# Kernel optimization log

Measured on AMD Instinct MI355X. Metric: run time of the kernel, lower is better.

Reference implementation:

```python
import jax, jax.numpy as jnp
import numpy as np
from jax import lax

DIM = 192
HEADS = 4
HIDDEN = int(DIM * 2.66)  # 510
B, H, W = 2, 64, 64
EPS_LN = 1e-6
EPS_NORM = 1e-12


def conv1x1(x, w, b):
    # x: (b,c,h,w), w: (o,c), b: (o,)
    return jnp.einsum('bchw,oc->bohw', x, w) + b[None, :, None, None]


def dwconv3x3(x, w, b):
    # depthwise 3x3, SAME padding; w: (C,1,3,3)
    c = x.shape[1]
    y = lax.conv_general_dilated(x, w, window_strides=(1, 1), padding='SAME',
                                 feature_group_count=c,
                                 dimension_numbers=('NCHW', 'OIHW', 'NCHW'))
    return y + b[None, :, None, None]


def layernorm2d(x, w, b):
    mean = jnp.mean(x, axis=(2, 3), keepdims=True)
    var = jnp.mean((x - mean) ** 2, axis=(2, 3), keepdims=True)
    return (x - mean) / jnp.sqrt(var + EPS_LN) * w[None, :, None, None] + b[None, :, None, None]


def mdta(x, qkv_w, qkv_b, qkv_dw_w, qkv_dw_b, temperature, proj_w, proj_b):
    b, c, h, w = x.shape
    qkv = dwconv3x3(conv1x1(x, qkv_w, qkv_b), qkv_dw_w, qkv_dw_b)
    q, k, v = jnp.split(qkv, 3, axis=1)
    dh = c // HEADS
    q = q.reshape(b, HEADS, dh, h * w)
    k = k.reshape(b, HEADS, dh, h * w)
    v = v.reshape(b, HEADS, dh, h * w)
    # L2-normalize over per-head channel dim (axis=2), like F.normalize(dim=2)
    q = q / jnp.maximum(jnp.linalg.norm(q, axis=2, keepdims=True), EPS_NORM)
    k = k / jnp.maximum(jnp.linalg.norm(k, axis=2, keepdims=True), EPS_NORM)
    # spatial attention map: (b, heads, HW, HW)
    attn = jnp.einsum('bhcn,bhcm->bhnm', q, k) * temperature[None]  # temp (heads,1,1)
    attn = jax.nn.softmax(attn, axis=-1)
    out = jnp.einsum('bhnm,bhcm->bhcn', attn, v)  # (b,heads,dh,HW)
    out = out.reshape(b, c, h, w)
    return conv1x1(out, proj_w, proj_b)


def gdfn(x, pin_w, pin_b, dw_w, dw_b, pout_w, pout_b):
    y = dwconv3x3(conv1x1(x, pin_w, pin_b), dw_w, dw_b)
    y1, y2 = jnp.split(y, 2, axis=1)
    y = jax.nn.gelu(y1, approximate=False) * y2
    return conv1x1(y, pout_w, pout_b)


def setup_inputs() -> dict:
    key = jax.random.key(0)
    ks = jax.random.split(key, 8)
    s = 0.02
    return {
        'x': jax.random.normal(ks[0], (B, DIM, H, W), jnp.float32),
        'ln1_w': jnp.ones((DIM,), jnp.float32),
        'ln1_b': jnp.zeros((DIM,), jnp.float32),
        'qkv_w': jax.random.normal(ks[1], (DIM * 3, DIM), jnp.float32) * s,
        'qkv_b': jnp.zeros((DIM * 3,), jnp.float32),
        'qkv_dw_w': jax.random.normal(ks[2], (DIM * 3, 1, 3, 3), jnp.float32) * s,
        'qkv_dw_b': jnp.zeros((DIM * 3,), jnp.float32),
        'temperature': jnp.ones((HEADS, 1, 1), jnp.float32),
        'proj_w': jax.random.normal(ks[3], (DIM, DIM), jnp.float32) * s,
        'proj_b': jnp.zeros((DIM,), jnp.float32),
        'ln2_w': jnp.ones((DIM,), jnp.float32),
        'ln2_b': jnp.zeros((DIM,), jnp.float32),
        'pin_w': jax.random.normal(ks[4], (HIDDEN * 2, DIM), jnp.float32) * s,
        'pin_b': jnp.zeros((HIDDEN * 2,), jnp.float32),
        'gdfn_dw_w': jax.random.normal(ks[5], (HIDDEN * 2, 1, 3, 3), jnp.float32) * s,
        'gdfn_dw_b': jnp.zeros((HIDDEN * 2,), jnp.float32),
        'pout_w': jax.random.normal(ks[6], (DIM, HIDDEN), jnp.float32) * s,
        'pout_b': jnp.zeros((DIM,), jnp.float32),
    }


def reference(x, ln1_w, ln1_b, qkv_w, qkv_b, qkv_dw_w, qkv_dw_b, temperature,
              proj_w, proj_b, ln2_w, ln2_b, pin_w, pin_b, gdfn_dw_w, gdfn_dw_b,
              pout_w, pout_b):
    x = x + mdta(layernorm2d(x, ln1_w, ln1_b), qkv_w, qkv_b, qkv_dw_w, qkv_dw_b,
                 temperature, proj_w, proj_b)
    x = x + gdfn(layernorm2d(x, ln2_w, ln2_b), pin_w, pin_b, gdfn_dw_w, gdfn_dw_b,
                 pout_w, pout_b)
    return x
```

## Files before the change

### kernel.cpp

```cpp
#include <hip/hip_runtime.h>
#include <hip/hip_bf16.h>

typedef __bf16 bf16x8 __attribute__((ext_vector_type(8)));
typedef __bf16 bf16x4 __attribute__((ext_vector_type(4)));
typedef __bf16 bf16x2 __attribute__((ext_vector_type(2)));
typedef float f32x4 __attribute__((ext_vector_type(4)));

#define HW 4096
#define DIMC 192
#define DH 48
#define HIDC 510
#define LOG2E 1.44269504088896f

__global__ void wcvt4_kernel(const float* __restrict__ qkv_w, const float* __restrict__ proj_w,
                             const float* __restrict__ pin_w, const float* __restrict__ pout_w,
                             __bf16* __restrict__ wb_qkv, __bf16* __restrict__ wb_proj,
                             __bf16* __restrict__ wb_pin, __bf16* __restrict__ wb_pout) {
  int idx = blockIdx.x * 256 + threadIdx.x;
  if (idx < 110592) {
    wb_qkv[idx] = (__bf16)qkv_w[idx];
  } else if (idx < 147456) {
    int i = idx - 110592;
    wb_proj[i] = (__bf16)proj_w[i];
  } else if (idx < 343296) {
    int i = idx - 147456;
    wb_pin[i] = (__bf16)pin_w[i];
  } else if (idx < 441600) {
    int i = idx - 343296;
    int o = i >> 9, c = i & 511;
    wb_pout[i] = (c < HIDC) ? (__bf16)pout_w[o * HIDC + c] : (__bf16)0.f;
  }
}

__global__ __launch_bounds__(256) void ln_stats_kernel(const float* __restrict__ x, const float* __restrict__ w,
                                                       const float* __restrict__ b, float* __restrict__ sc,
                                                       float* __restrict__ sh) {
  int bc = blockIdx.x;
  int c = bc % DIMC;
  const float* row = x + (size_t)bc * HW;
  float s = 0.f, s2 = 0.f;
  for (int i = threadIdx.x * 4; i < HW; i += 1024) {
    f32x4 v = *(const f32x4*)&row[i];
    s += (v.x + v.y) + (v.z + v.w);
    s2 = fmaf(v.x, v.x, s2); s2 = fmaf(v.y, v.y, s2);
    s2 = fmaf(v.z, v.z, s2); s2 = fmaf(v.w, v.w, s2);
  }
  __shared__ float red[8];
  for (int off = 32; off; off >>= 1) { s += __shfl_down(s, off, 64); s2 += __shfl_down(s2, off, 64); }
  int wid = threadIdx.x >> 6;
  if ((threadIdx.x & 63) == 0) { red[wid] = s; red[4 + wid] = s2; }
  __syncthreads();
  if (threadIdx.x == 0) {
    s = red[0] + red[1] + red[2] + red[3];
    s2 = red[4] + red[5] + red[6] + red[7];
    float mean = s * (1.f / HW);
    float var = s2 * (1.f / HW) - mean * mean;
    float rstd = rsqrtf(var + 1e-6f);
    float scv = rstd * w[c];
    sc[bc] = scv;
    sh[bc] = b[c] - mean * scv;
  }
}

__global__ __launch_bounds__(256) void ln_apply_t_kernel(const float* __restrict__ x, const float* __restrict__ sc,
                                                         const float* __restrict__ sh, __bf16* __restrict__ Xt) {
  int n0 = blockIdx.x * 64, c0 = blockIdx.y * 32, b = blockIdx.z;
  int t = threadIdx.x;
  int n = t & 63, cs = c0 + (t >> 6) * 8;
  __bf16 ob[8];
#pragma unroll
  for (int cc = 0; cc < 8; ++cc) {
    int c = cs + cc;
    float v = fmaf(x[((size_t)(b * DIMC + c)) * HW + n0 + n], sc[b * DIMC + c], sh[b * DIMC + c]);
    ob[cc] = (__bf16)v;
  }
  *(bf16x8*)&Xt[((size_t)((b << 12) + n0 + n)) * DIMC + cs] = *(bf16x8*)ob;
}

__global__ __launch_bounds__(256) void gemm_kernel(const __bf16* __restrict__ A, const __bf16* __restrict__ Bt,
                                                   const float* __restrict__ bias, const float* __restrict__ res,
                                                   float* __restrict__ outf, __bf16* __restrict__ outb,
                                                   int O, int Cs, int mode) {
  __shared__ __align__(16) __bf16 Asub[64 * 72];
  __shared__ __align__(16) __bf16 Bsub[128 * 72];
  const int t = threadIdx.x;
  const int lane = t & 63, wv = t >> 6;
  const int q4 = lane >> 4, l16 = lane & 15;
  int o0 = blockIdx.y * 64;
  if (o0 + 64 > O) o0 = O - 64;
  const int ntot0 = blockIdx.x * 128;
  const int b = ntot0 >> 12;
  const int n_in_b0 = ntot0 & 4095;

  f32x4 acc[8];
#pragma unroll
  for (int nt = 0; nt < 8; ++nt) acc[nt] = (f32x4){0.f, 0.f, 0.f, 0.f};

  for (int c0 = 0; c0 < Cs; c0 += 64) {
    __syncthreads();
#pragma unroll
    for (int j = 0; j < 2; ++j) {
      int id = t + 256 * j;
      *(bf16x8*)&Asub[(id >> 3) * 72 + (id & 7) * 8] =
          *(const bf16x8*)&A[((size_t)(o0 + (id >> 3))) * Cs + c0 + (id & 7) * 8];
    }
    if (mode != 3) {
#pragma unroll
      for (int j = 0; j < 4; ++j) {
        int id = t + 256 * j;
        *(bf16x8*)&Bsub[(id >> 3) * 72 + (id & 7) * 8] =
            *(const bf16x8*)&Bt[((size_t)(ntot0 + (id >> 3))) * Cs + c0 + (id & 7) * 8];
      }
    } else {
      int cr = t >> 2, seg = t & 3;
      int cg = c0 + cr;
      __bf16 tmp[32];
      if (cg < HIDC) {
        const __bf16* gp = Bt + ((size_t)(b * HIDC + cg)) * HW + n_in_b0 + seg * 32;
#pragma unroll
        for (int j = 0; j < 4; ++j) *(bf16x8*)&tmp[8 * j] = *(const bf16x8*)&gp[8 * j];
      } else {
#pragma unroll
        for (int k = 0; k < 32; ++k) tmp[k] = (__bf16)0.f;
      }
#pragma unroll
      for (int k = 0; k < 32; ++k) Bsub[(seg * 32 + k) * 72 + cr] = tmp[k];
    }
    __syncthreads();
#pragma unroll
    for (int ks = 0; ks < 2; ++ks) {
      bf16x8 af = *(const bf16x8*)&Asub[(16 * wv + l16) * 72 + 32 * ks + 8 * q4];
#pragma unroll
      for (int nt = 0; nt < 8; ++nt) {
        bf16x8 bfr = *(const bf16x8*)&Bsub[(16 * nt + l16) * 72 + 32 * ks + 8 * q4];
        acc[nt] = __builtin_amdgcn_mfma_f32_16x16x32_bf16(af, bfr, acc[nt], 0, 0, 0);
      }
    }
  }

  float bvals[4];
#pragma unroll
  for (int r = 0; r < 4; ++r) bvals[r] = bias[o0 + 16 * wv + 4 * q4 + r];
#pragma unroll
  for (int nt = 0; nt < 8; ++nt) {
    int n_in_b = n_in_b0 + 16 * nt + l16;
#pragma unroll
    for (int r = 0; r < 4; ++r) {
      int o = o0 + 16 * wv + 4 * q4 + r;
      size_t addr = ((size_t)(b * O + o)) * HW + n_in_b;
      float v = acc[nt][r] + bvals[r];
      if (mode >= 2) { outf[addr] = v + res[addr]; }
      else if (mode == 0) { outf[addr] = v; }
      else { outb[addr] = (__bf16)v; }
    }
  }
}

__global__ __launch_bounds__(256) void dwconv_split_kernel(const __bf16* __restrict__ in, const float* __restrict__ w,
                                                           const float* __restrict__ bias,
                                                           __bf16* __restrict__ qdwb, __bf16* __restrict__ Vbf) {
  int bc = blockIdx.x;
  int b = bc / 576, ch = bc - b * 576;
  __shared__ float tile[66 * 68];
  for (int i = threadIdx.x; i < 66 * 68; i += 256) tile[i] = 0.f;
  __syncthreads();
  const __bf16* p = in + (size_t)bc * HW;
  for (int j = 0; j < 8; ++j) {
    int i = 2 * threadIdx.x + 512 * j;
    bf16x2 v = *(const bf16x2*)&p[i];
    int y = i >> 6, xx = i & 63;
    tile[(y + 1) * 68 + xx + 1] = (float)v.x;
    tile[(y + 1) * 68 + xx + 2] = (float)v.y;
  }
  __syncthreads();
  float w0 = w[ch * 9 + 0], w1 = w[ch * 9 + 1], w2 = w[ch * 9 + 2];
  float w3 = w[ch * 9 + 3], w4 = w[ch * 9 + 4], w5 = w[ch * 9 + 5];
  float w6 = w[ch * 9 + 6], w7 = w[ch * 9 + 7], w8 = w[ch * 9 + 8];
  float bb = bias[ch];
  __bf16* dst;
  if (ch < 384) dst = qdwb + ((size_t)(b * 384 + ch)) * HW;
  else {
    int c = ch - 384, h = c / DH, cc = c - h * DH;
    dst = Vbf + ((size_t)((b * 4 + h) * DH + cc)) * HW;
  }
  for (int j = 0; j < 8; ++j) {
    int i = 2 * threadIdx.x + 512 * j;
    int y = i >> 6, xx = i & 63;
    const float* tt = &tile[y * 68 + xx];
    float a = bb;
    a = fmaf(w0, tt[0], a);   a = fmaf(w1, tt[1], a);   a = fmaf(w2, tt[2], a);
    a = fmaf(w3, tt[68], a);  a = fmaf(w4, tt[69], a);  a = fmaf(w5, tt[70], a);
    a = fmaf(w6, tt[136], a); a = fmaf(w7, tt[137], a); a = fmaf(w8, tt[138], a);
    float a2 = bb;
    a2 = fmaf(w0, tt[1], a2);   a2 = fmaf(w1, tt[2], a2);   a2 = fmaf(w2, tt[3], a2);
    a2 = fmaf(w3, tt[69], a2);  a2 = fmaf(w4, tt[70], a2);  a2 = fmaf(w5, tt[71], a2);
    a2 = fmaf(w6, tt[137], a2); a2 = fmaf(w7, tt[138], a2); a2 = fmaf(w8, tt[139], a2);
    bf16x2 o = { (__bf16)a, (__bf16)a2 };
    *(bf16x2*)&dst[i] = o;
  }
}

__global__ __launch_bounds__(256) void gdfn_dw_gate_kernel(const __bf16* __restrict__ hid, const float* __restrict__ w,
                                                           const float* __restrict__ bias, __bf16* __restrict__ gate) {
  int blk = blockIdx.x;
  int b = blk / HIDC, j = blk - b * HIDC;
  __shared__ float t1[66 * 68];
  __shared__ float t2[66 * 68];
  for (int i = threadIdx.x; i < 66 * 68; i += 256) { t1[i] = 0.f; t2[i] = 0.f; }
  __syncthreads();
  const __bf16* p1 = hid + ((size_t)b * (2 * HIDC) + j) * HW;
  const __bf16* p2 = p1 + (size_t)HIDC * HW;
  for (int jj = 0; jj < 8; ++jj) {
    int i = 2 * threadIdx.x + 512 * jj;
    bf16x2 v1 = *(const bf16x2*)&p1[i];
    bf16x2 v2 = *(const bf16x2*)&p2[i];
    int y = i >> 6, xx = i & 63;
    t1[(y + 1) * 68 + xx + 1] = (float)v1.x;
    t1[(y + 1) * 68 + xx + 2] = (float)v1.y;
    t2[(y + 1) * 68 + xx + 1] = (float)v2.x;
    t2[(y + 1) * 68 + xx + 2] = (float)v2.y;
  }
  __syncthreads();
  int c1 = j, c2 = j + HIDC;
  float a0 = w[c1*9+0], a1w = w[c1*9+1], a2w = w[c1*9+2], a3 = w[c1*9+3], a4 = w[c1*9+4],
        a5 = w[c1*9+5], a6 = w[c1*9+6], a7 = w[c1*9+7], a8 = w[c1*9+8];
  float b0 = w[c2*9+0], b1 = w[c2*9+1], b2 = w[c2*9+2], b3 = w[c2*9+3], b4 = w[c2*9+4],
        b5 = w[c2*9+5], b6 = w[c2*9+6], b7 = w[c2*9+7], b8 = w[c2*9+8];
  float bi1 = bias[c1], bi2 = bias[c2];
  __bf16* op = gate + ((size_t)b * HIDC + j) * HW;
  for (int jj = 0; jj < 8; ++jj) {
    int i = 2 * threadIdx.x + 512 * jj;
    int y = i >> 6, xx = i & 63;
    const float* u = &t1[y * 68 + xx];
    const float* v = &t2[y * 68 + xx];
    float x1 = bi1;
    x1 = fmaf(a0, u[0], x1);   x1 = fmaf(a1w, u[1], x1);  x1 = fmaf(a2w, u[2], x1);
    x1 = fmaf(a3, u[68], x1);  x1 = fmaf(a4, u[69], x1);  x1 = fmaf(a5, u[70], x1);
    x1 = fmaf(a6, u[136], x1); x1 = fmaf(a7, u[137], x1); x1 = fmaf(a8, u[138], x1);
    float x1b = bi1;
    x1b = fmaf(a0, u[1], x1b);   x1b = fmaf(a1w, u[2], x1b);  x1b = fmaf(a2w, u[3], x1b);
    x1b = fmaf(a3, u[69], x1b);  x1b = fmaf(a4, u[70], x1b);  x1b = fmaf(a5, u[71], x1b);
    x1b = fmaf(a6, u[137], x1b); x1b = fmaf(a7, u[138], x1b); x1b = fmaf(a8, u[139], x1b);
    float x2 = bi2;
    x2 = fmaf(b0, v[0], x2);   x2 = fmaf(b1, v[1], x2);   x2 = fmaf(b2, v[2], x2);
    x2 = fmaf(b3, v[68], x2);  x2 = fmaf(b4, v[69], x2);  x2 = fmaf(b5, v[70], x2);
    x2 = fmaf(b6, v[136], x2); x2 = fmaf(b7, v[137], x2); x2 = fmaf(b8, v[138], x2);
    float x2b = bi2;
    x2b = fmaf(b0, v[1], x2b);   x2b = fmaf(b1, v[2], x2b);   x2b = fmaf(b2, v[3], x2b);
    x2b = fmaf(b3, v[69], x2b);  x2b = fmaf(b4, v[70], x2b);  x2b = fmaf(b5, v[71], x2b);
    x2b = fmaf(b6, v[137], x2b); x2b = fmaf(b7, v[138], x2b); x2b = fmaf(b8, v[139], x2b);
    float g  = 0.5f * x1  * (1.f + erff(x1  * 0.70710678118654752f));
    float gb = 0.5f * x1b * (1.f + erff(x1b * 0.70710678118654752f));
    bf16x2 o = { (__bf16)(g * x2), (__bf16)(gb * x2b) };
    *(bf16x2*)&op[i] = o;
  }
}

__global__ __launch_bounds__(256) void prep_qk_kernel(const __bf16* __restrict__ qdwb, const float* __restrict__ temp,
                                                      __bf16* __restrict__ Qbf, __bf16* __restrict__ Kbf) {
  int t2 = blockIdx.x * 256 + threadIdx.x;
  int bh = t2 >> 11;
  int np = (t2 & 2047) * 2;
  int b = bh >> 2, h = bh & 3;
  const __bf16* qp = qdwb + ((size_t)(b * 384 + h * DH)) * HW + np;
  const __bf16* kp = qp + (size_t)192 * HW;
  float tq = temp[h] * LOG2E;

  bf16x2 raw[DH];
  float ss0 = 0.f, ss1 = 0.f;
#pragma unroll
  for (int c = 0; c < DH; ++c) {
    bf16x2 v = *(const bf16x2*)&qp[(size_t)c * HW];
    raw[c] = v;
    float f0 = (float)v.x, f1 = (float)v.y;
    ss0 = fmaf(f0, f0, ss0);
    ss1 = fmaf(f1, f1, ss1);
  }
  float sc0 = tq / fmaxf(sqrtf(ss0), 1e-12f);
  float sc1 = tq / fmaxf(sqrtf(ss1), 1e-12f);
  __bf16 ob0[64], ob1[64];
#pragma unroll
  for (int c = 0; c < DH; ++c) {
    ob0[c] = (__bf16)((float)raw[c].x * sc0);
    ob1[c] = (__bf16)((float)raw[c].y * sc1);
  }
#pragma unroll
  for (int c = DH; c < 64; ++c) { ob0[c] = (__bf16)0.f; ob1[c] = (__bf16)0.f; }
  __bf16* qd = Qbf + ((size_t)(bh << 12) + np) * 64;
#pragma unroll
  for (int ch = 0; ch < 8; ++ch) {
    *(bf16x8*)&qd[ch * 8] = *(bf16x8*)&ob0[ch * 8];
    *(bf16x8*)&qd[64 + ch * 8] = *(bf16x8*)&ob1[ch * 8];
  }

  ss0 = 0.f; ss1 = 0.f;
#pragma unroll
  for (int c = 0; c < DH; ++c) {
    bf16x2 v = *(const bf16x2*)&kp[(size_t)c * HW];
    raw[c] = v;
    float f0 = (float)v.x, f1 = (float)v.y;
    ss0 = fmaf(f0, f0, ss0);
    ss1 = fmaf(f1, f1, ss1);
  }
  sc0 = 1.f / fmaxf(sqrtf(ss0), 1e-12f);
  sc1 = 1.f / fmaxf(sqrtf(ss1), 1e-12f);
#pragma unroll
  for (int c = 0; c < DH; ++c) {
    ob0[c] = (__bf16)((float)raw[c].x * sc0);
    ob1[c] = (__bf16)((float)raw[c].y * sc1);
  }
  __bf16* kd = Kbf + ((size_t)(bh << 12) + np) * 64;
#pragma unroll
  for (int ch = 0; ch < 8; ++ch) {
    *(bf16x8*)&kd[ch * 8] = *(bf16x8*)&ob0[ch * 8];
    *(bf16x8*)&kd[64 + ch * 8] = *(bf16x8*)&ob1[ch * 8];
  }
}

__global__ __launch_bounds__(256) void attn_split_kernel(const __bf16* __restrict__ Qbf, const __bf16* __restrict__ Kbf,
                                                         const __bf16* __restrict__ Vbf, float* __restrict__ part) {
  __shared__ __align__(16) __bf16 Kt[64 * 72];
  __shared__ __align__(16) __bf16 Vc[48 * 72];
  __shared__ __align__(16) __bf16 Pl[64 * 72];
  const int tid = threadIdx.x;
  const int lane = tid & 63;
  const int wv = tid >> 6;
  const int q4 = lane >> 4, l16 = lane & 15;
  const int bid = blockIdx.x;
  const int chunk = bid >> 9, rest = bid & 511;
  const int bh = rest >> 6, nt = rest & 63;
  const int n0 = nt * 64;
  const __bf16* Qg = Qbf + (size_t)bh * HW * 64;
  const __bf16* Kg = Kbf + (size_t)bh * HW * 64;
  const __bf16* Vg = Vbf + (size_t)bh * DH * HW;

  bf16x8 qf[4][2];
#pragma unroll
  for (int s = 0; s < 4; ++s)
#pragma unroll
    for (int ks = 0; ks < 2; ++ks)
      qf[s][ks] = *(const bf16x8*)&Qg[((size_t)(n0 + 16 * s + l16)) * 64 + 32 * ks + 8 * q4];

  bf16x8 kreg[2], vreg[2];
  {
    const int m0 = chunk * 16 * 64;
#pragma unroll
    for (int j = 0; j < 2; ++j) {
      int id = tid + 256 * j;
      kreg[j] = *(const bf16x8*)&Kg[((size_t)(m0 + (id >> 3))) * 64 + (id & 7) * 8];
    }
    vreg[0] = *(const bf16x8*)&Vg[((size_t)(tid >> 3)) * HW + m0 + (tid & 7) * 8];
    if (tid < 128) {
      int i = tid + 256;
      vreg[1] = *(const bf16x8*)&Vg[((size_t)(i >> 3)) * HW + m0 + (i & 7) * 8];
    }
  }

  float lsub[4] = {0.f, 0.f, 0.f, 0.f};
  f32x4 oacc[3];
#pragma unroll
  for (int ct = 0; ct < 3; ++ct) oacc[ct] = (f32x4){0.f, 0.f, 0.f, 0.f};

  const int mt_end = chunk * 16 + 16;
  for (int mt = chunk * 16; mt < mt_end; ++mt) {
    __syncthreads();
#pragma unroll
    for (int j = 0; j < 2; ++j) {
      int id = tid + 256 * j;
      *(bf16x8*)&Kt[(id >> 3) * 72 + (id & 7) * 8] = kreg[j];
    }
    *(bf16x8*)&Vc[(tid >> 3) * 72 + (tid & 7) * 8] = vreg[0];
    if (tid < 128) {
      int i = tid + 256;
      *(bf16x8*)&Vc[(i >> 3) * 72 + (i & 7) * 8] = vreg[1];
    }
    if (mt + 1 < mt_end) {
      const int m1 = (mt + 1) * 64;
#pragma unroll
      for (int j = 0; j < 2; ++j) {
        int id = tid + 256 * j;
        kreg[j] = *(const bf16x8*)&Kg[((size_t)(m1 + (id >> 3))) * 64 + (id & 7) * 8];
      }
      vreg[0] = *(const bf16x8*)&Vg[((size_t)(tid >> 3)) * HW + m1 + (tid & 7) * 8];
      if (tid < 128) {
        int i = tid + 256;
        vreg[1] = *(const bf16x8*)&Vg[((size_t)(i >> 3)) * HW + m1 + (i & 7) * 8];
      }
    }
    __syncthreads();

    f32x4 sacc[4];
#pragma unroll
    for (int s = 0; s < 4; ++s) sacc[s] = (f32x4){0.f, 0.f, 0.f, 0.f};
#pragma unroll
    for (int ks = 0; ks < 2; ++ks) {
      bf16x8 af = *(const bf16x8*)&Kt[(16 * wv + l16) * 72 + 32 * ks + 8 * q4];
#pragma unroll
      for (int s = 0; s < 4; ++s)
        sacc[s] = __builtin_amdgcn_mfma_f32_16x16x32_bf16(af, qf[s][ks], sacc[s], 0, 0, 0);
    }

#pragma unroll
    for (int s = 0; s < 4; ++s) {
      float p0 = exp2f(sacc[s][0]);
      float p1 = exp2f(sacc[s][1]);
      float p2 = exp2f(sacc[s][2]);
      float p3 = exp2f(sacc[s][3]);
      lsub[s] += (p0 + p1) + (p2 + p3);
      bf16x4 pk = { (__bf16)p0, (__bf16)p1, (__bf16)p2, (__bf16)p3 };
      *(bf16x4*)&Pl[(16 * s + l16) * 72 + 16 * wv + 4 * q4] = pk;
    }
    __syncthreads();

#pragma unroll
    for (int ks = 0; ks < 2; ++ks) {
      bf16x8 pf = *(const bf16x8*)&Pl[(16 * wv + l16) * 72 + 32 * ks + 8 * q4];
#pragma unroll
      for (int ct = 0; ct < 3; ++ct) {
        bf16x8 vf = *(const bf16x8*)&Vc[(16 * ct + l16) * 72 + 32 * ks + 8 * q4];
        oacc[ct] = __builtin_amdgcn_mfma_f32_16x16x32_bf16(pf, vf, oacc[ct], 0, 0, 0);
      }
    }
  }

  __syncthreads();
  float* Lred = (float*)Kt;
#pragma unroll
  for (int s = 0; s < 4; ++s) {
    float v = lsub[s];
    v += __shfl_xor(v, 16, 64);
    v += __shfl_xor(v, 32, 64);
    if (q4 == 0) Lred[wv * 64 + 16 * s + l16] = v;
  }
  __syncthreads();
  size_t pbase = (size_t)bid * 3136;
  if (tid < 64)
    part[pbase + 3072 + tid] = Lred[tid] + Lred[64 + tid] + Lred[128 + tid] + Lred[192 + tid];
#pragma unroll
  for (int ct = 0; ct < 3; ++ct)
#pragma unroll
    for (int r = 0; r < 4; ++r) {
      int n = 16 * wv + 4 * q4 + r;
      part[pbase + (size_t)n * 48 + 16 * ct + l16] = oacc[ct][r];
    }
}

__global__ __launch_bounds__(256) void attn_merge_kernel(const float* __restrict__ part, __bf16* __restrict__ Xt) {
  const int bid = blockIdx.x;
  const int bh = bid >> 6, nt = bid & 63;
  const int b = bh >> 2, h = bh & 3;
  const int n0 = nt * 64;
  const int t = threadIdx.x;
  __shared__ float linv[64];
  if (t < 64) {
    float s = 0.f;
#pragma unroll
    for (int ch = 0; ch < 4; ++ch) s += part[((size_t)(ch * 512 + bid)) * 3136 + 3072 + t];
    linv[t] = 1.f / s;
  }
  __syncthreads();
#pragma unroll
  for (int j = 0; j < 3; ++j) {
    int id = t + 256 * j;
    int n = id / 12, cc = (id - n * 12) * 4;
    f32x4 s = (f32x4){0.f, 0.f, 0.f, 0.f};
#pragma unroll
    for (int ch = 0; ch < 4; ++ch) s += *(const f32x4*)&part[((size_t)(ch * 512 + bid)) * 3136 + (size_t)n * 48 + cc];
    float li = linv[n];
    bf16x4 ov = { (__bf16)(s.x * li), (__bf16)(s.y * li), (__bf16)(s.z * li), (__bf16)(s.w * li) };
    *(bf16x4*)&Xt[((size_t)((b << 12) + n0 + n)) * DIMC + h * DH + cc] = ov;
  }
}

extern "C" void kernel_launch(void* const* d_in, const int* in_sizes, int n_in,
                              void* d_out, int out_size, void* d_ws, size_t ws_size,
                              hipStream_t stream) {
  const float* x        = (const float*)d_in[0];
  const float* ln1_w    = (const float*)d_in[1];
  const float* ln1_b    = (const float*)d_in[2];
  const float* qkv_w    = (const float*)d_in[3];
  const float* qkv_b    = (const float*)d_in[4];
  const float* qkv_dw_w = (const float*)d_in[5];
  const float* qkv_dw_b = (const float*)d_in[6];
  const float* temperature = (const float*)d_in[7];
  const float* proj_w   = (const float*)d_in[8];
  const float* proj_b   = (const float*)d_in[9];
  const float* ln2_w    = (const float*)d_in[10];
  const float* ln2_b    = (const float*)d_in[11];
  const float* pin_w    = (const float*)d_in[12];
  const float* pin_b    = (const float*)d_in[13];
  const float* gdfn_dw_w = (const float*)d_in[14];
  const float* gdfn_dw_b = (const float*)d_in[15];
  const float* pout_w   = (const float*)d_in[16];
  const float* pout_b   = (const float*)d_in[17];
  float* out = (float*)d_out;
  float* ws = (float*)d_ws;

  __bf16* wb_qkv  = (__bf16*)(ws + 0);
  __bf16* wb_proj = (__bf16*)(ws + 55296);
  __bf16* wb_pin  = (__bf16*)(ws + 73728);
  __bf16* wb_pout = (__bf16*)(ws + 171648);
  float* sc1 = ws + 220800;
  float* sh1 = ws + 221184;
  float* sc2 = ws + 221568;
  float* sh2 = ws + 221952;
  __bf16* Xt1 = (__bf16*)(ws + 222336);
  __bf16* Xt2 = (__bf16*)(ws + 222336);
  __bf16* Qbf = (__bf16*)(ws + 222336);
  __bf16* Kbf = (__bf16*)(ws + 1270912);
  __bf16* Vbf = (__bf16*)(ws + 2319488);
  __bf16* qkvb   = (__bf16*)(ws + 3105920);
  __bf16* Xt_att = (__bf16*)(ws + 3105920);
  __bf16* hid    = (__bf16*)(ws + 3105920);
  __bf16* qdwb  = (__bf16*)(ws + 5465216);
  float*  Opart = ws + 5465216;
  __bf16* gate  = (__bf16*)(ws + 7283840);

  wcvt4_kernel<<<1725, 256, 0, stream>>>(qkv_w, proj_w, pin_w, pout_w, wb_qkv, wb_proj, wb_pin, wb_pout);

  ln_stats_kernel<<<2 * DIMC, 256, 0, stream>>>(x, ln1_w, ln1_b, sc1, sh1);
  ln_apply_t_kernel<<<dim3(64, 6, 2), 256, 0, stream>>>(x, sc1, sh1, Xt1);
  gemm_kernel<<<dim3(64, 9), 256, 0, stream>>>(wb_qkv, Xt1, qkv_b, nullptr, nullptr, qkvb, 576, 192, 1);
  dwconv_split_kernel<<<1152, 256, 0, stream>>>(qkvb, qkv_dw_w, qkv_dw_b, qdwb, Vbf);
  prep_qk_kernel<<<64, 256, 0, stream>>>(qdwb, temperature, Qbf, Kbf);
  attn_split_kernel<<<2048, 256, 0, stream>>>(Qbf, Kbf, Vbf, Opart);
  attn_merge_kernel<<<512, 256, 0, stream>>>(Opart, Xt_att);
  gemm_kernel<<<dim3(64, 3), 256, 0, stream>>>(wb_proj, Xt_att, proj_b, x, out, nullptr, 192, 192, 2);

  ln_stats_kernel<<<2 * DIMC, 256, 0, stream>>>(out, ln2_w, ln2_b, sc2, sh2);
  ln_apply_t_kernel<<<dim3(64, 6, 2), 256, 0, stream>>>(out, sc2, sh2, Xt2);
  gemm_kernel<<<dim3(64, 16), 256, 0, stream>>>(wb_pin, Xt2, pin_b, nullptr, nullptr, hid, 1020, 192, 1);
  gdfn_dw_gate_kernel<<<2 * HIDC, 256, 0, stream>>>(hid, gdfn_dw_w, gdfn_dw_b, gate);
  gemm_kernel<<<dim3(64, 3), 256, 0, stream>>>(wb_pout, (const __bf16*)gate, pout_b, out, out, nullptr, 192, 512, 3);
}
```

Baseline: 260.1 us.

## Widen attention key tiles to 128 and fold row sums into PV MFMA

The split-attention kernel now processes 128 keys per iteration (8 iterations instead of 16), halving the barrier count per chunk. It appends a row of ones to the V tile so a fourth MFMA column computes the softmax denominator, replacing the separate exp-sum accumulation and cross-wave shuffle reduction. It also adds s_setprio around the MFMA phases and changes the thread mapping of the mode-3 transpose load in the GEMM so consecutive threads handle consecutive channels. The cost is more LDS, extra PV MFMA work for the ones column, and more registers held in flight.

```diff
diff --git a/kernel.cpp b/kernel.cpp
--- a/kernel.cpp
+++ b/kernel.cpp
@@ -112,7 +112,7 @@
             *(const bf16x8*)&Bt[((size_t)(ntot0 + (id >> 3))) * Cs + c0 + (id & 7) * 8];
       }
     } else {
-      int cr = t >> 2, seg = t & 3;
+      int cr = t & 63, seg = t >> 6;
       int cg = c0 + cr;
       __bf16 tmp[32];
       if (cg < HIDC) {
@@ -319,9 +319,9 @@
 
 __global__ __launch_bounds__(256) void attn_split_kernel(const __bf16* __restrict__ Qbf, const __bf16* __restrict__ Kbf,
                                                          const __bf16* __restrict__ Vbf, float* __restrict__ part) {
-  __shared__ __align__(16) __bf16 Kt[64 * 72];
-  __shared__ __align__(16) __bf16 Vc[48 * 72];
-  __shared__ __align__(16) __bf16 Pl[64 * 72];
+  __shared__ __align__(16) __bf16 Kt[128 * 72];
+  __shared__ __align__(16) __bf16 Vc[64 * 136];
+  __shared__ __align__(16) __bf16 Pl[64 * 136];
   const int tid = threadIdx.x;
   const int lane = tid & 63;
   const int wv = tid >> 6;
@@ -341,101 +341,96 @@
     for (int ks = 0; ks < 2; ++ks)
       qf[s][ks] = *(const bf16x8*)&Qg[((size_t)(n0 + 16 * s + l16)) * 64 + 32 * ks + 8 * q4];
 
-  bf16x8 kreg[2], vreg[2];
-  {
-    const int m0 = chunk * 16 * 64;
-#pragma unroll
-    for (int j = 0; j < 2; ++j) {
-      int id = tid + 256 * j;
-      kreg[j] = *(const bf16x8*)&Kg[((size_t)(m0 + (id >> 3))) * 64 + (id & 7) * 8];
-    }
-    vreg[0] = *(const bf16x8*)&Vg[((size_t)(tid >> 3)) * HW + m0 + (tid & 7) * 8];
-    if (tid < 128) {
-      int i = tid + 256;
-      vreg[1] = *(const bf16x8*)&Vg[((size_t)(i >> 3)) * HW + m0 + (i & 7) * 8];
-    }
-  }
-
-  float lsub[4] = {0.f, 0.f, 0.f, 0.f};
-  f32x4 oacc[3];
-#pragma unroll
-  for (int ct = 0; ct < 3; ++ct) oacc[ct] = (f32x4){0.f, 0.f, 0.f, 0.f};
-
-  const int mt_end = chunk * 16 + 16;
-  for (int mt = chunk * 16; mt < mt_end; ++mt) {
+  for (int i = tid; i < 16 * 136; i += 256)
+    Vc[48 * 136 + i] = (i < 136) ? (__bf16)1.f : (__bf16)0.f;
+
+  bf16x8 kreg[4], vreg[3];
+  const int mbase0 = chunk * 1024;
+#pragma unroll
+  for (int j = 0; j < 4; ++j) {
+    int id = tid + 256 * j;
+    kreg[j] = *(const bf16x8*)&Kg[((size_t)(mbase0 + (id >> 3))) * 64 + (id & 7) * 8];
+  }
+#pragma unroll
+  for (int j = 0; j < 3; ++j) {
+    int id = tid + 256 * j;
+    vreg[j] = *(const bf16x8*)&Vg[((size_t)(id >> 4)) * HW + mbase0 + (id & 15) * 8];
+  }
+
+  f32x4 oacc[4];
+#pragma unroll
+  for (int ct = 0; ct < 4; ++ct) oacc[ct] = (f32x4){0.f, 0.f, 0.f, 0.f};
+
+  for (int it = 0; it < 8; ++it) {
     __syncthreads();
 #pragma unroll
-    for (int j = 0; j < 2; ++j) {
+    for (int j = 0; j < 4; ++j) {
       int id = tid + 256 * j;
       *(bf16x8*)&Kt[(id >> 3) * 72 + (id & 7) * 8] = kreg[j];
     }
-    *(bf16x8*)&Vc[(tid >> 3) * 72 + (tid & 7) * 8] = vreg[0];
-    if (tid < 128) {
-      int i = tid + 256;
-      *(bf16x8*)&Vc[(i >> 3) * 72 + (i & 7) * 8] = vreg[1];
-    }
-    if (mt + 1 < mt_end) {
-      const int m1 = (mt + 1) * 64;
-#pragma unroll
-      for (int j = 0; j < 2; ++j) {
+#pragma unroll
+    for (int j = 0; j < 3; ++j) {
+      int id = tid + 256 * j;
+      *(bf16x8*)&Vc[(id >> 4) * 136 + (id & 15) * 8] = vreg[j];
+    }
+    if (it < 7) {
+      const int m1 = mbase0 + (it + 1) * 128;
+#pragma unroll
+      for (int j = 0; j < 4; ++j) {
         int id = tid + 256 * j;
         kreg[j] = *(const bf16x8*)&Kg[((size_t)(m1 + (id >> 3))) * 64 + (id & 7) * 8];
       }
-      vreg[0] = *(const bf16x8*)&Vg[((size_t)(tid >> 3)) * HW + m1 + (tid & 7) * 8];
-      if (tid < 128) {
-        int i = tid + 256;
-        vreg[1] = *(const bf16x8*)&Vg[((size_t)(i >> 3)) * HW + m1 + (i & 7) * 8];
+#pragma unroll
+      for (int j = 0; j < 3; ++j) {
+        int id = tid + 256 * j;
+        vreg[j] = *(const bf16x8*)&Vg[((size_t)(id >> 4)) * HW + m1 + (id & 15) * 8];
       }
     }
     __syncthreads();
 
-    f32x4 sacc[4];
-#pragma unroll
-    for (int s = 0; s < 4; ++s) sacc[s] = (f32x4){0.f, 0.f, 0.f, 0.f};
-#pragma unroll
-    for (int ks = 0; ks < 2; ++ks) {
-      bf16x8 af = *(const bf16x8*)&Kt[(16 * wv + l16) * 72 + 32 * ks + 8 * q4];
-#pragma unroll
-      for (int s = 0; s < 4; ++s)
-        sacc[s] = __builtin_amdgcn_mfma_f32_16x16x32_bf16(af, qf[s][ks], sacc[s], 0, 0, 0);
-    }
-
-#pragma unroll
-    for (int s = 0; s < 4; ++s) {
-      float p0 = exp2f(sacc[s][0]);
-      float p1 = exp2f(sacc[s][1]);
-      float p2 = exp2f(sacc[s][2]);
-      float p3 = exp2f(sacc[s][3]);
-      lsub[s] += (p0 + p1) + (p2 + p3);
-      bf16x4 pk = { (__bf16)p0, (__bf16)p1, (__bf16)p2, (__bf16)p3 };
-      *(bf16x4*)&Pl[(16 * s + l16) * 72 + 16 * wv + 4 * q4] = pk;
-    }
+    f32x4 sacc[2][4];
+#pragma unroll
+    for (int g = 0; g < 2; ++g)
+#pragma unroll
+      for (int s = 0; s < 4; ++s) sacc[g][s] = (f32x4){0.f, 0.f, 0.f, 0.f};
+    __builtin_amdgcn_s_setprio(1);
+#pragma unroll
+    for (int g = 0; g < 2; ++g) {
+      const int r0 = 16 * (wv + 4 * g);
+#pragma unroll
+      for (int ks = 0; ks < 2; ++ks) {
+        bf16x8 af = *(const bf16x8*)&Kt[(r0 + l16) * 72 + 32 * ks + 8 * q4];
+#pragma unroll
+        for (int s = 0; s < 4; ++s)
+          sacc[g][s] = __builtin_amdgcn_mfma_f32_16x16x32_bf16(af, qf[s][ks], sacc[g][s], 0, 0, 0);
+      }
+    }
+    __builtin_amdgcn_s_setprio(0);
+
+#pragma unroll
+    for (int g = 0; g < 2; ++g)
+#pragma unroll
+      for (int s = 0; s < 4; ++s) {
+        bf16x4 pk = { (__bf16)exp2f(sacc[g][s][0]), (__bf16)exp2f(sacc[g][s][1]),
+                      (__bf16)exp2f(sacc[g][s][2]), (__bf16)exp2f(sacc[g][s][3]) };
+        *(bf16x4*)&Pl[(16 * s + l16) * 136 + 16 * (wv + 4 * g) + 4 * q4] = pk;
+      }
     __syncthreads();
 
-#pragma unroll
-    for (int ks = 0; ks < 2; ++ks) {
-      bf16x8 pf = *(const bf16x8*)&Pl[(16 * wv + l16) * 72 + 32 * ks + 8 * q4];
-#pragma unroll
-      for (int ct = 0; ct < 3; ++ct) {
-        bf16x8 vf = *(const bf16x8*)&Vc[(16 * ct + l16) * 72 + 32 * ks + 8 * q4];
+    __builtin_amdgcn_s_setprio(1);
+#pragma unroll
+    for (int ks = 0; ks < 4; ++ks) {
+      bf16x8 pf = *(const bf16x8*)&Pl[(16 * wv + l16) * 136 + 32 * ks + 8 * q4];
+#pragma unroll
+      for (int ct = 0; ct < 4; ++ct) {
+        bf16x8 vf = *(const bf16x8*)&Vc[(16 * ct + l16) * 136 + 32 * ks + 8 * q4];
         oacc[ct] = __builtin_amdgcn_mfma_f32_16x16x32_bf16(pf, vf, oacc[ct], 0, 0, 0);
       }
     }
-  }
-
-  __syncthreads();
-  float* Lred = (float*)Kt;
-#pragma unroll
-  for (int s = 0; s < 4; ++s) {
-    float v = lsub[s];
-    v += __shfl_xor(v, 16, 64);
-    v += __shfl_xor(v, 32, 64);
-    if (q4 == 0) Lred[wv * 64 + 16 * s + l16] = v;
-  }
-  __syncthreads();
+    __builtin_amdgcn_s_setprio(0);
+  }
+
   size_t pbase = (size_t)bid * 3136;
-  if (tid < 64)
-    part[pbase + 3072 + tid] = Lred[tid] + Lred[64 + tid] + Lred[128 + tid] + Lred[192 + tid];
 #pragma unroll
   for (int ct = 0; ct < 3; ++ct)
 #pragma unroll
@@ -443,6 +438,11 @@
       int n = 16 * wv + 4 * q4 + r;
       part[pbase + (size_t)n * 48 + 16 * ct + l16] = oacc[ct][r];
     }
+  if (l16 == 0) {
+#pragma unroll
+    for (int r = 0; r < 4; ++r)
+      part[pbase + 3072 + 16 * wv + 4 * q4 + r] = oacc[3][r];
+  }
 }
 
 __global__ __launch_bounds__(256) void attn_merge_kernel(const float* __restrict__ part, __bf16* __restrict__ Xt) {
```

Result: slower. 270.4 us (+4.0%).
